# Kernel optimization log

Measured on AMD Instinct MI355X. Metric: run time of the kernel, lower is better.

The kernel has to match this reference:

```python
import jax, jax.numpy as jnp
import numpy as np

N_NODES = 200000
N_EDGES = 1000000
N_GRAPHS = 4096
F_IN = 11
H = 64


def setup_inputs() -> dict:
    key = jax.random.key(0)
    ks = jax.random.split(key, 8)
    x = jax.random.normal(ks[0], (N_NODES, F_IN), jnp.float32)
    edge_index = jax.random.randint(ks[1], (2, N_EDGES), 0, N_NODES, jnp.int32)
    batch = jnp.sort(jax.random.randint(ks[2], (N_NODES,), 0, N_GRAPHS, jnp.int32))
    def glorot(k, shape):
        fan_in, fan_out = shape[0], shape[1]
        s = jnp.sqrt(6.0 / (fan_in + fan_out))
        return jax.random.uniform(k, shape, jnp.float32, -s, s)
    return {
        "x": x,
        "edge_index": edge_index,
        "batch": batch,
        "W1": glorot(ks[3], (F_IN, H)),
        "b1": jnp.zeros((H,), jnp.float32),
        "W2": glorot(ks[4], (H, H)),
        "b2": jnp.zeros((H,), jnp.float32),
        "W3": glorot(ks[5], (H, H)),
        "b3": jnp.zeros((H,), jnp.float32),
        "lin_w": glorot(ks[6], (H, 1)),
        "lin_b": jnp.zeros((1,), jnp.float32),
    }


def _gcn_conv(x, W, b, src, dst, norm, num_nodes):
    # linear transform then gather-scale-scatter (PyG GCNConv, source_to_target)
    h = x @ W                                   # [N, out]
    msg = h[src] * norm[:, None]                # [E+N, out]
    out = jax.ops.segment_sum(msg, dst, num_segments=num_nodes)
    return out + b


def reference(x, edge_index, batch, W1, b1, W2, b2, W3, b3, lin_w, lin_b):
    n = x.shape[0]
    # add self-loops (gcn_norm with add_self_loops=True)
    loops = jnp.arange(n, dtype=edge_index.dtype)
    src = jnp.concatenate([edge_index[0], loops])
    dst = jnp.concatenate([edge_index[1], loops])
    deg = jax.ops.segment_sum(jnp.ones_like(dst, x.dtype), dst, num_segments=n)
    dis = jnp.where(deg > 0, jax.lax.rsqrt(jnp.maximum(deg, 1.0)), 0.0)
    norm = dis[src] * dis[dst]                  # symmetric normalization

    h = jax.nn.relu(_gcn_conv(x, W1, b1, src, dst, norm, n))
    h = jax.nn.relu(_gcn_conv(h, W2, b2, src, dst, norm, n))
    h = _gcn_conv(h, W3, b3, src, dst, norm, n)  # no relu after conv3

    # global mean pool over graph ids
    sums = jax.ops.segment_sum(h, batch, num_segments=N_GRAPHS)
    cnts = jax.ops.segment_sum(jnp.ones((n,), h.dtype), batch, num_segments=N_GRAPHS)
    pooled = sums / jnp.maximum(cnts, 1.0)[:, None]
    # dropout is identity in eval mode
    return pooled @ lin_w + lin_b
```

## Files before the change

kernel.cpp:

```cpp
#include <hip/hip_runtime.h>
#include <hip/hip_fp16.h>

#define N_NODES 200000
#define N_EDGES 1000000
#define N_GRAPHS 4096
#define F_IN 11
#define H 64
#define XP 16


__global__ void deg_kernel(const int* __restrict__ dst, int* __restrict__ deg) {
    int i = blockIdx.x * blockDim.x + threadIdx.x;
    if (i < N_EDGES) atomicAdd(&deg[dst[i]], 1);
}

__global__ void batch_cnt_kernel(const int* __restrict__ batch, int* __restrict__ cnts) {
    int i = blockIdx.x * blockDim.x + threadIdx.x;
    if (i < N_NODES) atomicAdd(&cnts[batch[i]], 1);
}


__global__ void scan_block_kernel(const int* __restrict__ deg, int* __restrict__ ex,
                                  int* __restrict__ bsum, float* __restrict__ dis) {
    __shared__ int sh[256];
    int i = blockIdx.x * 256 + threadIdx.x;
    int v = (i < N_NODES) ? deg[i] : 0;
    if (i < N_NODES) dis[i] = rsqrtf((float)(v + 1));
    sh[threadIdx.x] = v;
    __syncthreads();
    for (int o = 1; o < 256; o <<= 1) {
        int t = (threadIdx.x >= o) ? sh[threadIdx.x - o] : 0;
        __syncthreads();
        sh[threadIdx.x] += t;
        __syncthreads();
    }
    if (i < N_NODES) ex[i] = sh[threadIdx.x] - v;
    if (threadIdx.x == 255) bsum[blockIdx.x] = sh[255];
}

__global__ void scan_top_kernel(int* __restrict__ bsum, int nb) {
    __shared__ int sh[1024];
    int v = ((int)threadIdx.x < nb) ? bsum[threadIdx.x] : 0;
    sh[threadIdx.x] = v;
    __syncthreads();
    for (int o = 1; o < 1024; o <<= 1) {
        int t = ((int)threadIdx.x >= o) ? sh[threadIdx.x - o] : 0;
        __syncthreads();
        sh[threadIdx.x] += t;
        __syncthreads();
    }
    if ((int)threadIdx.x < nb) bsum[threadIdx.x] = sh[threadIdx.x] - v;
}

__global__ void scan_add_kernel(const int* __restrict__ ex, const int* __restrict__ boff,
                                int* __restrict__ row_start, int* __restrict__ cursor) {
    int i = blockIdx.x * 256 + threadIdx.x;
    if (i >= N_NODES) return;
    int r = ex[i] + boff[i >> 8];
    row_start[i] = r;
    cursor[i] = r;
    if (i == 0) row_start[N_NODES] = N_EDGES;
}

__global__ void place_kernel(const int* __restrict__ src, const int* __restrict__ dst,
                             int* __restrict__ cursor, int* __restrict__ csr) {
    int e = blockIdx.x * blockDim.x + threadIdx.x;
    if (e < N_EDGES) {
        int p = atomicAdd(&cursor[dst[e]], 1);
        csr[p] = src[e];
    }
}


__global__ void w3l_kernel(const float* __restrict__ W3, const float* __restrict__ lw,
                           float* __restrict__ w3l) {
    int k = threadIdx.x;
    if (k < H) {
        float s = 0.f;
#pragma unroll
        for (int j = 0; j < H; ++j) s += W3[k * H + j] * lw[j];
        w3l[k] = s;
    }
}


__global__ void xscale_kernel(const float* __restrict__ x, const float* __restrict__ dis,
                              float* __restrict__ xs) {
    int i = blockIdx.x * blockDim.x + threadIdx.x;
    if (i < N_NODES * XP) {
        int row = i >> 4;
        int c = i & 15;
        xs[i] = (c < F_IN) ? x[(size_t)row * F_IN + c] * dis[row] : 0.f;
    }
}


__global__ void gather1_kernel(const int* __restrict__ row_start, const int* __restrict__ csr,
                               const float* __restrict__ xs, const float* __restrict__ dis,
                               float* __restrict__ P) {
    int lane = threadIdx.x & 63;
    int c = lane & 15;
    int u = lane >> 4;
    int wave = (blockIdx.x * blockDim.x + threadIdx.x) >> 6;
    int nw = (gridDim.x * blockDim.x) >> 6;
    for (int n4 = wave * 4; n4 < N_NODES; n4 += nw * 4) {
        int n = n4 + u;
        int e0 = row_start[n], e1 = row_start[n + 1];
        float acc = xs[(size_t)n * XP + c];
        int e = e0;
        for (; e + 4 <= e1; e += 4) {
            int s0 = csr[e], s1 = csr[e + 1], s2 = csr[e + 2], s3 = csr[e + 3];
            float v0 = xs[(size_t)s0 * XP + c];
            float v1 = xs[(size_t)s1 * XP + c];
            float v2 = xs[(size_t)s2 * XP + c];
            float v3 = xs[(size_t)s3 * XP + c];
            acc += (v0 + v1) + (v2 + v3);
        }
        for (; e < e1; ++e) acc += xs[(size_t)csr[e] * XP + c];
        P[(size_t)n * XP + c] = acc * dis[n];
    }
}


template <int K, bool HALF_OUT>
__global__ void gemm_tile_kernel(const float* __restrict__ X, const float* __restrict__ W,
                                 const float* __restrict__ dis, const float* __restrict__ bias,
                                 void* __restrict__ Y) {
    constexpr int KS = (K == F_IN) ? XP : K;
    __shared__ float Xt[KS][68];
    __shared__ float Ws[K][64];
    int tid = threadIdx.x;
    int rowbase = blockIdx.x * 64;

    for (int i = tid; i < K * 64; i += 256) Ws[i >> 6][i & 63] = W[i];

    if (K == 64) {
        for (int t = tid; t < 1024; t += 256) {
            int r = t >> 4;
            int kc = (t & 15) * 4;
            float4 v = *(const float4*)(X + (size_t)(rowbase + r) * 64 + kc);
            Xt[kc + 0][r] = v.x;
            Xt[kc + 1][r] = v.y;
            Xt[kc + 2][r] = v.z;
            Xt[kc + 3][r] = v.w;
        }
    } else {
        int r = tid >> 2;
        int c4 = (tid & 3) * 4;
        float4 v = *(const float4*)(X + (size_t)(rowbase + r) * XP + c4);
        Xt[c4 + 0][r] = v.x;
        Xt[c4 + 1][r] = v.y;
        Xt[c4 + 2][r] = v.z;
        Xt[c4 + 3][r] = v.w;
    }
    __syncthreads();

    int tc = (tid & 15) * 4;
    int tr = (tid >> 4) * 4;
    float a00 = 0, a01 = 0, a02 = 0, a03 = 0;
    float a10 = 0, a11 = 0, a12 = 0, a13 = 0;
    float a20 = 0, a21 = 0, a22 = 0, a23 = 0;
    float a30 = 0, a31 = 0, a32 = 0, a33 = 0;
#pragma unroll
    for (int k = 0; k < K; ++k) {
        float4 xv = *(const float4*)&Xt[k][tr];
        float4 wv = *(const float4*)&Ws[k][tc];
        a00 += xv.x * wv.x; a01 += xv.x * wv.y; a02 += xv.x * wv.z; a03 += xv.x * wv.w;
        a10 += xv.y * wv.x; a11 += xv.y * wv.y; a12 += xv.y * wv.z; a13 += xv.y * wv.w;
        a20 += xv.z * wv.x; a21 += xv.z * wv.y; a22 += xv.z * wv.z; a23 += xv.z * wv.w;
        a30 += xv.w * wv.x; a31 += xv.w * wv.y; a32 += xv.w * wv.z; a33 += xv.w * wv.w;
    }
    float acc[4][4] = {{a00, a01, a02, a03}, {a10, a11, a12, a13},
                       {a20, a21, a22, a23}, {a30, a31, a32, a33}};
    float4 bv = {0, 0, 0, 0};
    if (!HALF_OUT) bv = *(const float4*)(bias + tc);
#pragma unroll
    for (int i = 0; i < 4; ++i) {
        int row = rowbase + tr + i;
        if (HALF_OUT) {
            float d = dis[row];
            union { uint2 u; __half2 h[2]; } pk;
            pk.h[0] = __floats2half2_rn(acc[i][0] * d, acc[i][1] * d);
            pk.h[1] = __floats2half2_rn(acc[i][2] * d, acc[i][3] * d);
            *(uint2*)((__half*)Y + (size_t)row * 64 + tc) = pk.u;
        } else {
            float4 o;
            o.x = fmaxf(acc[i][0] + bv.x, 0.f);
            o.y = fmaxf(acc[i][1] + bv.y, 0.f);
            o.z = fmaxf(acc[i][2] + bv.z, 0.f);
            o.w = fmaxf(acc[i][3] + bv.w, 0.f);
            *(float4*)((float*)Y + (size_t)row * 64 + tc) = o;
        }
    }
}


__global__ void gather_fused_kernel(const int* __restrict__ row_start,
                                    const int* __restrict__ csr,
                                    const __half* __restrict__ Bsh,
                                    const float* __restrict__ dis,
                                    const float* __restrict__ b2,
                                    const float* __restrict__ w3l,
                                    float* __restrict__ y) {
    int lane = threadIdx.x & 63;
    int q = lane & 15;
    int g = lane >> 4;
    int wave = (blockIdx.x * blockDim.x + threadIdx.x) >> 6;
    int nw = (gridDim.x * blockDim.x) >> 6;
    float4 bi = ((const float4*)b2)[q];
    float4 wl = ((const float4*)w3l)[q];
    for (int n = wave; n < N_NODES; n += nw) {
        int e0 = row_start[n], e1 = row_start[n + 1];
        int nslots = e1 - e0 + 1;
        float4 acc = {0.f, 0.f, 0.f, 0.f};
        for (int base = 0; base < nslots; base += 4) {
            int slot = base + g;
            if (slot < nslots) {
                int s = (slot == 0) ? n : csr[e0 + slot - 1];
                union { uint2 u; __half2 h[2]; } r;
                r.u = *(const uint2*)(Bsh + (size_t)s * 64 + q * 4);
                float2 f0 = __half22float2(r.h[0]);
                float2 f1 = __half22float2(r.h[1]);
                acc.x += f0.x; acc.y += f0.y; acc.z += f1.x; acc.w += f1.y;
            }
        }
#pragma unroll
        for (int m = 16; m <= 32; m <<= 1) {
            acc.x += __shfl_xor(acc.x, m, 64);
            acc.y += __shfl_xor(acc.y, m, 64);
            acc.z += __shfl_xor(acc.z, m, 64);
            acc.w += __shfl_xor(acc.w, m, 64);
        }
        if (g == 0) {
            float d = dis[n];
            float ox = fmaxf(acc.x * d + bi.x, 0.f);
            float oy = fmaxf(acc.y * d + bi.y, 0.f);
            float oz = fmaxf(acc.z * d + bi.z, 0.f);
            float ow = fmaxf(acc.w * d + bi.w, 0.f);
            float p = ox * wl.x + oy * wl.y + oz * wl.z + ow * wl.w;
#pragma unroll
            for (int m = 1; m <= 8; m <<= 1) p += __shfl_xor(p, m, 64);
            if (q == 0) y[n] = p * d;
        }
    }
}


__global__ void pool_scalar_kernel(const int* __restrict__ row_start,
                                   const int* __restrict__ csr,
                                   const float* __restrict__ y,
                                   const float* __restrict__ dis,
                                   const int* __restrict__ batch,
                                   float* __restrict__ gsum) {
    int n = blockIdx.x * blockDim.x + threadIdx.x;
    if (n >= N_NODES) return;
    int e0 = row_start[n], e1 = row_start[n + 1];
    float s = y[n];
    int e = e0;
    for (; e + 4 <= e1; e += 4) {
        float v0 = y[csr[e]], v1 = y[csr[e + 1]], v2 = y[csr[e + 2]], v3 = y[csr[e + 3]];
        s += (v0 + v1) + (v2 + v3);
    }
    for (; e < e1; ++e) s += y[csr[e]];
    atomicAdd(&gsum[batch[n]], s * dis[n]);
}


__global__ void head2_kernel(const float* __restrict__ gsum, const int* __restrict__ cnts,
                             const float* __restrict__ b3, const float* __restrict__ lw,
                             const float* __restrict__ lb, float* __restrict__ out) {
    int g = blockIdx.x * blockDim.x + threadIdx.x;
    if (g >= N_GRAPHS) return;
    float cb = 0.f;
#pragma unroll
    for (int k = 0; k < H; ++k) cb += b3[k] * lw[k];
    int c = cnts[g];
    out[g] = (c > 0) ? (gsum[g] / (float)c + cb + lb[0]) : lb[0];
}

extern "C" void kernel_launch(void* const* d_in, const int* in_sizes, int n_in,
                              void* d_out, int out_size, void* d_ws, size_t ws_size,
                              hipStream_t stream) {
    const float* x     = (const float*)d_in[0];
    const int*   ei    = (const int*)d_in[1];
    const int*   batch = (const int*)d_in[2];
    const float* W1    = (const float*)d_in[3];
    const float* b1    = (const float*)d_in[4];
    const float* W2    = (const float*)d_in[5];
    const float* b2    = (const float*)d_in[6];
    const float* W3    = (const float*)d_in[7];
    const float* b3    = (const float*)d_in[8];
    const float* lw    = (const float*)d_in[9];
    const float* lb    = (const float*)d_in[10];
    float* out = (float*)d_out;

    const int* src = ei;
    const int* dst = ei + N_EDGES;

    const size_t NH = (size_t)N_NODES * H;
    char* ws = (char*)d_ws;
    float*  A         = (float*)ws;
    char*   Bregion   = ws + NH * 4;
    __half* Bsh       = (__half*)Bregion;
    float*  dis       = (float*)(ws + 2 * NH * 4);
    int*    row_start = (int*)(ws + 2 * NH * 4 + (size_t)N_NODES * 4);
    int*    csr       = (int*)((char*)row_start + ((size_t)N_NODES + 1) * 4);
    float*  gsum      = (float*)((char*)csr + (size_t)N_EDGES * 4);
    int*    cnts      = (int*)((char*)gsum + (size_t)N_GRAPHS * 4);
    float*  w3l       = (float*)((char*)cnts + (size_t)N_GRAPHS * 4);
    float*  y = A;
    float* xs = (float*)Bregion;
    float* P  = (float*)(Bregion + (16u << 20));
    int* deg    = (int*)A;
    int* ex     = (int*)((char*)A + (size_t)N_NODES * 4);
    int* cursor = (int*)((char*)A + 2 * (size_t)N_NODES * 4);
    int* bsum   = (int*)((char*)A + 3 * (size_t)N_NODES * 4);

    const int BT = 256;
    const int NB_NODES = (N_NODES + 255) / 256;
    const int gemm_grid = N_NODES / 64;
    const int gath_grid = 2048;

    hipMemsetAsync(deg, 0, (size_t)N_NODES * 4, stream);
    hipMemsetAsync(gsum, 0, (size_t)N_GRAPHS * 8, stream);
    deg_kernel<<<(N_EDGES + BT - 1) / BT, BT, 0, stream>>>(dst, deg);
    batch_cnt_kernel<<<NB_NODES, BT, 0, stream>>>(batch, cnts);
    scan_block_kernel<<<NB_NODES, 256, 0, stream>>>(deg, ex, bsum, dis);
    scan_top_kernel<<<1, 1024, 0, stream>>>(bsum, NB_NODES);
    scan_add_kernel<<<NB_NODES, 256, 0, stream>>>(ex, bsum, row_start, cursor);
    place_kernel<<<(N_EDGES + BT - 1) / BT, BT, 0, stream>>>(src, dst, cursor, csr);
    w3l_kernel<<<1, 64, 0, stream>>>(W3, lw, w3l);

    xscale_kernel<<<(N_NODES * XP + BT - 1) / BT, BT, 0, stream>>>(x, dis, xs);
    gather1_kernel<<<gath_grid, BT, 0, stream>>>(row_start, csr, xs, dis, P);
    gemm_tile_kernel<F_IN, false><<<gemm_grid, BT, 0, stream>>>(P, W1, dis, b1, A);

    gemm_tile_kernel<H, true><<<gemm_grid, BT, 0, stream>>>(A, W2, dis, b2, Bsh);
    gather_fused_kernel<<<gath_grid, BT, 0, stream>>>(row_start, csr, Bsh, dis, b2, w3l, y);

    pool_scalar_kernel<<<NB_NODES, BT, 0, stream>>>(row_start, csr, y, dis, batch, gsum);

    head2_kernel<<<(N_GRAPHS + BT - 1) / BT, BT, 0, stream>>>(gsum, cnts, b3, lw, lb, out);
}
```

Before: 421.3 us.

## Two-pass binned CSR build and edge-parallel gathers with wider vector loads

CSR construction becomes two passes. Edges are first binned by destination block (256 nodes per bin) into a staging buffer of (src,dst) pairs, then scattered to their final CSR slots, so the per-node atomics and csr writes land in a localized region. The layer-1 gather, the fused layer-2 gather and the pooling kernel now split each node's edge list across many lanes with wider loads (float4, uint4 of halves) and reduce with shuffles, instead of one lane group walking edges serially. This raises memory-level parallelism on short adjacency lists. It costs an extra kernel and a staging buffer of 8 MB, and it adds shuffle-reduction overhead and idle lanes when nodes have low degree.

Result: slower. 656.9 us (+55.9%).

```diff
diff --git a/kernel.cpp b/kernel.cpp
--- a/kernel.cpp
+++ b/kernel.cpp
@@ -53,21 +53,34 @@
 }
 
 __global__ void scan_add_kernel(const int* __restrict__ ex, const int* __restrict__ boff,
-                                int* __restrict__ row_start, int* __restrict__ cursor) {
+                                int* __restrict__ row_start, int* __restrict__ cursor,
+                                int* __restrict__ bcur) {
     int i = blockIdx.x * 256 + threadIdx.x;
     if (i >= N_NODES) return;
     int r = ex[i] + boff[i >> 8];
     row_start[i] = r;
     cursor[i] = r;
+    if ((i & 255) == 0) bcur[i >> 8] = r;
     if (i == 0) row_start[N_NODES] = N_EDGES;
 }
 
-__global__ void place_kernel(const int* __restrict__ src, const int* __restrict__ dst,
-                             int* __restrict__ cursor, int* __restrict__ csr) {
+__global__ void binA_kernel(const int* __restrict__ src, const int* __restrict__ dst,
+                            int* __restrict__ bcur, uint2* __restrict__ stage) {
     int e = blockIdx.x * blockDim.x + threadIdx.x;
     if (e < N_EDGES) {
-        int p = atomicAdd(&cursor[dst[e]], 1);
-        csr[p] = src[e];
+        int d = dst[e];
+        int p = atomicAdd(&bcur[d >> 8], 1);
+        stage[p] = make_uint2((unsigned)src[e], (unsigned)d);
+    }
+}
+
+__global__ void binB_kernel(const uint2* __restrict__ stage, int* __restrict__ cursor,
+                            int* __restrict__ csr) {
+    int i = blockIdx.x * blockDim.x + threadIdx.x;
+    if (i < N_EDGES) {
+        uint2 sd = stage[i];
+        int p = atomicAdd(&cursor[sd.y], 1);
+        csr[p] = (int)sd.x;
     }
 }
 
@@ -99,25 +112,35 @@
                                const float* __restrict__ xs, const float* __restrict__ dis,
                                float* __restrict__ P) {
     int lane = threadIdx.x & 63;
-    int c = lane & 15;
-    int u = lane >> 4;
+    int j = lane & 3;
+    int g = lane >> 2;
     int wave = (blockIdx.x * blockDim.x + threadIdx.x) >> 6;
     int nw = (gridDim.x * blockDim.x) >> 6;
-    for (int n4 = wave * 4; n4 < N_NODES; n4 += nw * 4) {
-        int n = n4 + u;
+    for (int n = wave; n < N_NODES; n += nw) {
         int e0 = row_start[n], e1 = row_start[n + 1];
-        float acc = xs[(size_t)n * XP + c];
-        int e = e0;
-        for (; e + 4 <= e1; e += 4) {
-            int s0 = csr[e], s1 = csr[e + 1], s2 = csr[e + 2], s3 = csr[e + 3];
-            float v0 = xs[(size_t)s0 * XP + c];
-            float v1 = xs[(size_t)s1 * XP + c];
-            float v2 = xs[(size_t)s2 * XP + c];
-            float v3 = xs[(size_t)s3 * XP + c];
-            acc += (v0 + v1) + (v2 + v3);
-        }
-        for (; e < e1; ++e) acc += xs[(size_t)csr[e] * XP + c];
-        P[(size_t)n * XP + c] = acc * dis[n];
+        int nslots = e1 - e0 + 1;
+        float4 acc = {0.f, 0.f, 0.f, 0.f};
+        for (int base = 0; base < nslots; base += 16) {
+            int slot = base + g;
+            if (slot < nslots) {
+                int s = (slot == 0) ? n : csr[e0 + slot - 1];
+                float4 v = *(const float4*)(xs + (size_t)s * XP + j * 4);
+                acc.x += v.x; acc.y += v.y; acc.z += v.z; acc.w += v.w;
+            }
+        }
+#pragma unroll
+        for (int m = 4; m <= 32; m <<= 1) {
+            acc.x += __shfl_xor(acc.x, m, 64);
+            acc.y += __shfl_xor(acc.y, m, 64);
+            acc.z += __shfl_xor(acc.z, m, 64);
+            acc.w += __shfl_xor(acc.w, m, 64);
+        }
+        if (g == 0) {
+            float d = dis[n];
+            float4 o;
+            o.x = acc.x * d; o.y = acc.y * d; o.z = acc.z * d; o.w = acc.w * d;
+            *(float4*)(P + (size_t)n * XP + j * 4) = o;
+        }
     }
 }
 
@@ -203,44 +226,49 @@
                                     const float* __restrict__ w3l,
                                     float* __restrict__ y) {
     int lane = threadIdx.x & 63;
-    int q = lane & 15;
-    int g = lane >> 4;
+    int j = lane & 7;
+    int g = lane >> 3;
     int wave = (blockIdx.x * blockDim.x + threadIdx.x) >> 6;
     int nw = (gridDim.x * blockDim.x) >> 6;
-    float4 bi = ((const float4*)b2)[q];
-    float4 wl = ((const float4*)w3l)[q];
+    float4 bi0 = *(const float4*)(b2 + j * 8);
+    float4 bi1 = *(const float4*)(b2 + j * 8 + 4);
+    float4 wl0 = *(const float4*)(w3l + j * 8);
+    float4 wl1 = *(const float4*)(w3l + j * 8 + 4);
     for (int n = wave; n < N_NODES; n += nw) {
         int e0 = row_start[n], e1 = row_start[n + 1];
         int nslots = e1 - e0 + 1;
-        float4 acc = {0.f, 0.f, 0.f, 0.f};
-        for (int base = 0; base < nslots; base += 4) {
+        float acc[8] = {0.f, 0.f, 0.f, 0.f, 0.f, 0.f, 0.f, 0.f};
+        for (int base = 0; base < nslots; base += 8) {
             int slot = base + g;
             if (slot < nslots) {
                 int s = (slot == 0) ? n : csr[e0 + slot - 1];
-                union { uint2 u; __half2 h[2]; } r;
-                r.u = *(const uint2*)(Bsh + (size_t)s * 64 + q * 4);
+                union { uint4 u; __half2 h[4]; } r;
+                r.u = *(const uint4*)(Bsh + (size_t)s * 64 + j * 8);
                 float2 f0 = __half22float2(r.h[0]);
                 float2 f1 = __half22float2(r.h[1]);
-                acc.x += f0.x; acc.y += f0.y; acc.z += f1.x; acc.w += f1.y;
+                float2 f2 = __half22float2(r.h[2]);
+                float2 f3 = __half22float2(r.h[3]);
+                acc[0] += f0.x; acc[1] += f0.y; acc[2] += f1.x; acc[3] += f1.y;
+                acc[4] += f2.x; acc[5] += f2.y; acc[6] += f3.x; acc[7] += f3.y;
             }
         }
 #pragma unroll
-        for (int m = 16; m <= 32; m <<= 1) {
-            acc.x += __shfl_xor(acc.x, m, 64);
-            acc.y += __shfl_xor(acc.y, m, 64);
-            acc.z += __shfl_xor(acc.z, m, 64);
-            acc.w += __shfl_xor(acc.w, m, 64);
+        for (int m = 8; m <= 32; m <<= 1) {
+#pragma unroll
+            for (int k = 0; k < 8; ++k) acc[k] += __shfl_xor(acc[k], m, 64);
         }
         if (g == 0) {
             float d = dis[n];
-            float ox = fmaxf(acc.x * d + bi.x, 0.f);
-            float oy = fmaxf(acc.y * d + bi.y, 0.f);
-            float oz = fmaxf(acc.z * d + bi.z, 0.f);
-            float ow = fmaxf(acc.w * d + bi.w, 0.f);
-            float p = ox * wl.x + oy * wl.y + oz * wl.z + ow * wl.w;
-#pragma unroll
-            for (int m = 1; m <= 8; m <<= 1) p += __shfl_xor(p, m, 64);
-            if (q == 0) y[n] = p * d;
+            float bi[8] = {bi0.x, bi0.y, bi0.z, bi0.w, bi1.x, bi1.y, bi1.z, bi1.w};
+            float wl[8] = {wl0.x, wl0.y, wl0.z, wl0.w, wl1.x, wl1.y, wl1.z, wl1.w};
+            float p = 0.f;
+#pragma unroll
+            for (int k = 0; k < 8; ++k)
+                p += fmaxf(acc[k] * d + bi[k], 0.f) * wl[k];
+            p += __shfl_xor(p, 1, 64);
+            p += __shfl_xor(p, 2, 64);
+            p += __shfl_xor(p, 4, 64);
+            if (j == 0) y[n] = p * d;
         }
     }
 }
@@ -252,17 +280,26 @@
                                    const float* __restrict__ dis,
                                    const int* __restrict__ batch,
                                    float* __restrict__ gsum) {
-    int n = blockIdx.x * blockDim.x + threadIdx.x;
-    if (n >= N_NODES) return;
+    int lane = threadIdx.x & 63;
+    int u = lane >> 4;
+    int t = lane & 15;
+    int wave = (blockIdx.x * blockDim.x + threadIdx.x) >> 6;
+    int n = wave * 4 + u;
     int e0 = row_start[n], e1 = row_start[n + 1];
-    float s = y[n];
-    int e = e0;
-    for (; e + 4 <= e1; e += 4) {
-        float v0 = y[csr[e]], v1 = y[csr[e + 1]], v2 = y[csr[e + 2]], v3 = y[csr[e + 3]];
-        s += (v0 + v1) + (v2 + v3);
-    }
-    for (; e < e1; ++e) s += y[csr[e]];
-    atomicAdd(&gsum[batch[n]], s * dis[n]);
+    int nslots = e1 - e0 + 1;
+    float acc = 0.f;
+    for (int base = 0; base < nslots; base += 16) {
+        int slot = base + t;
+        if (slot < nslots) {
+            int s = (slot == 0) ? n : csr[e0 + slot - 1];
+            acc += y[s];
+        }
+    }
+    acc += __shfl_xor(acc, 1, 64);
+    acc += __shfl_xor(acc, 2, 64);
+    acc += __shfl_xor(acc, 4, 64);
+    acc += __shfl_xor(acc, 8, 64);
+    if (t == 0) atomicAdd(&gsum[batch[n]], acc * dis[n]);
 }
 
 
@@ -308,9 +345,11 @@
     float*  gsum      = (float*)((char*)csr + (size_t)N_EDGES * 4);
     int*    cnts      = (int*)((char*)gsum + (size_t)N_GRAPHS * 4);
     float*  w3l       = (float*)((char*)cnts + (size_t)N_GRAPHS * 4);
+    int*    bcur      = (int*)((char*)w3l + 256);
     float*  y = A;
     float* xs = (float*)Bregion;
     float* P  = (float*)(Bregion + (16u << 20));
+    uint2* stage = (uint2*)(Bregion + (32u << 20));
     int* deg    = (int*)A;
     int* ex     = (int*)((char*)A + (size_t)N_NODES * 4);
     int* cursor = (int*)((char*)A + 2 * (size_t)N_NODES * 4);
@@ -327,8 +366,9 @@
     batch_cnt_kernel<<<NB_NODES, BT, 0, stream>>>(batch, cnts);
     scan_block_kernel<<<NB_NODES, 256, 0, stream>>>(deg, ex, bsum, dis);
     scan_top_kernel<<<1, 1024, 0, stream>>>(bsum, NB_NODES);
-    scan_add_kernel<<<NB_NODES, 256, 0, stream>>>(ex, bsum, row_start, cursor);
-    place_kernel<<<(N_EDGES + BT - 1) / BT, BT, 0, stream>>>(src, dst, cursor, csr);
+    scan_add_kernel<<<NB_NODES, 256, 0, stream>>>(ex, bsum, row_start, cursor, bcur);
+    binA_kernel<<<(N_EDGES + BT - 1) / BT, BT, 0, stream>>>(src, dst, bcur, stage);
+    binB_kernel<<<(N_EDGES + BT - 1) / BT, BT, 0, stream>>>(stage, cursor, csr);
     w3l_kernel<<<1, 64, 0, stream>>>(W3, lw, w3l);
 
     xscale_kernel<<<(N_NODES * XP + BT - 1) / BT, BT, 0, stream>>>(x, dis, xs);
@@ -338,7 +378,8 @@
     gemm_tile_kernel<H, true><<<gemm_grid, BT, 0, stream>>>(A, W2, dis, b2, Bsh);
     gather_fused_kernel<<<gath_grid, BT, 0, stream>>>(row_start, csr, Bsh, dis, b2, w3l, y);
 
-    pool_scalar_kernel<<<NB_NODES, BT, 0, stream>>>(row_start, csr, y, dis, batch, gsum);
+    pool_scalar_kernel<<<N_NODES / (4 * 4), BT, 0, stream>>>(row_start, csr, y, dis,
+                                                             batch, gsum);
 
     head2_kernel<<<(N_GRAPHS + BT - 1) / BT, BT, 0, stream>>>(gsum, cnts, b3, lw, lb, out);
 }
```
